# Performance work log

Measured on AMD Instinct MI355X. Metric: run time of the kernel, lower is better.

Reference implementation:

```python
import jax, jax.numpy as jnp
import numpy as np

CH, XH, YH, RADIUS = 2, 2, 2, 1  # channel_heads, x_heads, y_heads, neighborhood radius


def neighborhood_mask(n_sub_x, n_sub_y, radius):
    # clamped neighbor offsets reduce to |di|<=r and |dj|<=r within the grid
    iy = jnp.arange(n_sub_y)
    ix = jnp.arange(n_sub_x)
    my = jnp.abs(iy[:, None] - iy[None, :]) <= radius  # [ny, ny]
    mx = jnp.abs(ix[:, None] - ix[None, :]) <= radius  # [nx, nx]
    m = my[:, None, :, None] & mx[None, :, None, :]    # [ny, nx, ny, nx]
    s = n_sub_x * n_sub_y
    return m.reshape(s, s)  # row-major (h1 w1)(h2 w2), matching einops


def setup_inputs() -> dict:
    key = jax.random.key(0)
    k1, k2, k3 = jax.random.split(key, 3)
    C = 128
    seq = jax.random.normal(k1, (2, 256, C, 16, 16), dtype=jnp.float32)
    w_qkv = jax.random.normal(k2, (3 * C, C), dtype=jnp.float32) / np.sqrt(C).astype(np.float32)
    w_out = jax.random.normal(k3, (C, C), dtype=jnp.float32) / np.sqrt(C).astype(np.float32)
    b_out = jnp.zeros((C,), dtype=jnp.float32)
    return {"seq": seq, "w_qkv": w_qkv, "w_out": w_out, "b_out": b_out,
            "n_sub_x": 16, "n_sub_y": 16}


def reference(seq, w_qkv, w_out, b_out, n_sub_x, n_sub_y):
    b, s, C, H, W = seq.shape
    h, w = H // YH, W // XH
    c = C // CH
    nH = YH * XH * CH  # total heads

    # pointwise qkv projection over channels: [b, s, 3C, H, W]
    qkv = jnp.einsum('bschw,dc->bsdhw', seq, w_qkv)

    # decompose2d: split spatial grid into y_heads x x_heads blocks -> spatial heads
    # [b, s, 3C, YH, h, XH, w] -> [b, s, YH*XH, 3C, h, w]
    qkv = qkv.reshape(b, s, 3 * C, YH, h, XH, w)
    qkv = qkv.transpose(0, 1, 3, 5, 2, 4, 6).reshape(b, s, YH * XH, 3 * C, h, w)

    # split into q,k,v and channel heads: 3C = 3 * CH * c
    qkv = qkv.reshape(b, s, YH * XH, 3, CH, c, h, w)
    # -> [3, b, (spatial_heads * channel_heads), s, c, h, w]
    qkv = qkv.transpose(3, 0, 2, 4, 1, 5, 6, 7).reshape(3, b, nH, s, c, h, w)
    q, k, v = qkv[0], qkv[1], qkv[2]

    # scaled dot-product attention over flattened function dim (c,h,w)
    scale = 1.0 / np.sqrt(c * h * w).astype(np.float32)
    scores = jnp.einsum('bnschw,bntchw->bnst', q, k) * scale  # [b, nH, s, s]
    mask = neighborhood_mask(n_sub_x, n_sub_y, RADIUS)  # [s, s]
    scores = jnp.where(mask[None, None, :, :], scores, jnp.finfo(scores.dtype).min)
    attn = jax.nn.softmax(scores, axis=-1)
    sa = jnp.einsum('bnst,bntchw->bnschw', attn, v)  # [b, nH, s, c, h, w]

    # merge channel heads back: [b, s, spatial_heads, C, h, w]
    sa = sa.reshape(b, YH * XH, CH, s, c, h, w)
    sa = sa.transpose(0, 3, 1, 2, 4, 5, 6).reshape(b, s, YH, XH, C, h, w)
    # recompose2d: [b, s, C, H, W]
    sa = sa.transpose(0, 1, 4, 2, 5, 3, 6).reshape(b, s, C, H, W)

    # output pointwise projection with bias
    out = jnp.einsum('bschw,dc->bsdhw', sa, w_out) + b_out[None, None, :, None, None]
    return out
```

## Files before the change

kernel.cpp:

```cpp
#include <hip/hip_runtime.h>

#define BATCH 2
#define SS    256
#define CC    128
#define HWN   256
#define FDIM  4096

typedef unsigned int uint;
typedef unsigned short ushort;
typedef short bf16x8 __attribute__((ext_vector_type(8)));
typedef ushort us4 __attribute__((ext_vector_type(4)));
typedef float f32x4 __attribute__((ext_vector_type(4)));

__device__ __forceinline__ ushort f2b(float f) {
  uint u = __float_as_uint(f);
  return (ushort)((u + 0x7fffu + ((u >> 16) & 1u)) >> 16);
}
__device__ __forceinline__ float b2f(ushort h) { return __uint_as_float((uint)h << 16); }

__global__ void k_convert(const float* __restrict__ wqkv, const float* __restrict__ wout,
                          ushort* __restrict__ wqkv_b, ushort* __restrict__ wout_b) {
  int i = blockIdx.x * 256 + threadIdx.x;
  if (i < 384 * 128) wqkv_b[i] = f2b(wqkv[i]);
  if (i < 128 * 128) {
    const int cc = i & 127;
    const int ks = cc >> 5, qq = (cc >> 3) & 3, j = cc & 7;
    const int creal = (ks >> 1) * 64 + ((((ks & 1) << 1) | (qq >> 1)) << 4)
                      + ((qq & 1) << 3) + j;
    wout_b[i] = f2b(wout[(i >> 7) * 128 + creal]);
  }
}

__global__ __launch_bounds__(256, 2) void k_qkv(const float* __restrict__ seq,
                                                const ushort* __restrict__ wqkv_b,
                                                ushort* __restrict__ qkvh) {
  __shared__ ushort wlds[128 * 128];
  const int bs = blockIdx.x;
  const int b = bs >> 8, s = bs & 255;
  const int t = threadIdx.x;
  const int hq = t >> 6, lane = t & 63;
  const int qq = lane >> 4, m = lane & 15;

  const float* sp = seq + (size_t)bs * (CC * HWN);

  bf16x8 bfrag[4][4];
  uint obase[4];
  #pragma unroll
  for (int set = 0; set < 4; ++set) {
    const int ntg = hq * 4 + set;
    const int hw = ntg * 16 + m;
    #pragma unroll
    for (int ks = 0; ks < 4; ++ks) {
      const int k0 = ks * 32 + qq * 8;
      float tmp[8];
      #pragma unroll
      for (int j = 0; j < 8; ++j) tmp[j] = sp[(k0 + j) * HWN + hw];
      bf16x8 fr;
      #pragma unroll
      for (int j = 0; j < 8; ++j) fr[j] = (short)f2b(tmp[j]);
      bfrag[set][ks] = fr;
    }
    const int n_qk = ((ntg >> 3) * 2 + (m >> 3)) * 2;
    const int hwl  = (ntg & 7) * 8 + (m & 7);
    obase[set] = (uint)(((b * 8 + n_qk) * SS + s) * FDIM + hwl * 16 + qq * 4);
  }

  for (int qkvi = 0; qkvi < 3; ++qkvi) {
    if (qkvi) __syncthreads();
    #pragma unroll
    for (int i = 0; i < 8; ++i) {
      const int row = i * 16 + (t >> 4), col16 = t & 15;
      bf16x8 w = *(const bf16x8*)(wqkv_b + (qkvi * 128 + row) * 128 + col16 * 8);
      *(bf16x8*)&wlds[row * 128 + ((col16 ^ (row & 15)) * 8)] = w;
    }
    __syncthreads();

    #pragma unroll
    for (int mt8 = 0; mt8 < 8; ++mt8) {
      bf16x8 afrag[4];
      #pragma unroll
      for (int ks = 0; ks < 4; ++ks)
        afrag[ks] = *(const bf16x8*)&wlds[(mt8 * 16 + m) * 128 + (((ks * 4 + qq) ^ m) * 8)];
      const int ch = mt8 >> 2, m4 = mt8 & 3;
      #pragma unroll
      for (int set = 0; set < 4; ++set) {
        f32x4 acc = {0.f, 0.f, 0.f, 0.f};
        #pragma unroll
        for (int ks = 0; ks < 4; ++ks)
          acc = __builtin_amdgcn_mfma_f32_16x16x32_bf16(afrag[ks], bfrag[set][ks], acc, 0, 0, 0);
        us4 pk;
        #pragma unroll
        for (int r = 0; r < 4; ++r) pk[r] = f2b(acc[r]);
        *(us4*)(qkvh + obase[set]
                + (uint)((qkvi * 16 + ch) * (SS * FDIM) + m4 * 1024)) = pk;
      }
    }
  }
}

__global__ __launch_bounds__(1024) void k_scores(const ushort* __restrict__ qkvh,
                                                 float* __restrict__ attn) {
  __shared__ float red[16][64][12];
  const int g = blockIdx.x;
  const int unit = (g & 7) * 32 + (g >> 3);
  const int b  = unit >> 7;
  const int n  = (unit >> 4) & 7;
  const int sy = unit & 15;
  const int t = threadIdx.x;
  const int wave = t >> 6, lane = t & 63;
  const int qq = lane >> 4, l15 = lane & 15;
  const size_t hs = (size_t)SS * FDIM;
  const ushort* qb = qkvh + (size_t)(b * 8 + n) * hs;
  const ushort* kb = qkvh + (size_t)(16 + b * 8 + n) * hs;

  const ushort* qp = qb + (size_t)(sy * 16 + l15) * FDIM + qq * 8;
  const ushort* kp[3];
  #pragma unroll
  for (int tl = 0; tl < 3; ++tl) {
    const int tyc = min(max(sy - 1 + tl, 0), 15);
    kp[tl] = kb + (size_t)(tyc * 16 + l15) * FDIM + qq * 8;
  }

  f32x4 acc[3] = {{0,0,0,0},{0,0,0,0},{0,0,0,0}};
  const int kbeg = wave * 256;
  #pragma unroll
  for (int it = 0; it < 4; ++it) {
    const int k0 = kbeg + it * 64;
    bf16x8 a0 = *(const bf16x8*)(qp + k0);
    bf16x8 a1 = *(const bf16x8*)(qp + k0 + 32);
    bf16x8 b0[3], b1[3];
    #pragma unroll
    for (int tl = 0; tl < 3; ++tl) {
      b0[tl] = *(const bf16x8*)(kp[tl] + k0);
      b1[tl] = *(const bf16x8*)(kp[tl] + k0 + 32);
    }
    #pragma unroll
    for (int tl = 0; tl < 3; ++tl)
      acc[tl] = __builtin_amdgcn_mfma_f32_16x16x32_bf16(a0, b0[tl], acc[tl], 0, 0, 0);
    #pragma unroll
    for (int tl = 0; tl < 3; ++tl)
      acc[tl] = __builtin_amdgcn_mfma_f32_16x16x32_bf16(a1, b1[tl], acc[tl], 0, 0, 0);
  }

  #pragma unroll
  for (int tl = 0; tl < 3; ++tl)
    #pragma unroll
    for (int r = 0; r < 4; ++r) red[wave][lane][tl * 4 + r] = acc[tl][r];
  __syncthreads();
  if (t < 768) {
    const int lane2 = t / 12, idx = t - lane2 * 12;
    float ssum = red[0][lane2][idx];
    #pragma unroll
    for (int w = 1; w < 16; ++w) ssum += red[w][lane2][idx];
    red[0][lane2][idx] = ssum;
  }
  __syncthreads();
  if (wave != 0) return;
  #pragma unroll
  for (int tl = 0; tl < 3; ++tl)
    #pragma unroll
    for (int r = 0; r < 4; ++r) acc[tl][r] = red[0][lane][tl * 4 + r];

  const int tx = l15;
  float sc[3][4];
  #pragma unroll
  for (int tl = 0; tl < 3; ++tl) {
    const int ty = sy - 1 + tl;
    const bool tyv = (ty >= 0 && ty < 16);
    #pragma unroll
    for (int r = 0; r < 4; ++r) {
      const int sx = qq * 4 + r;
      const bool v = tyv && (tx - sx <= 1) && (sx - tx <= 1);
      sc[tl][r] = v ? acc[tl][r] * (1.f / 64.f) : -1e30f;
    }
  }
  #pragma unroll
  for (int r = 0; r < 4; ++r) {
    float mx = fmaxf(fmaxf(sc[0][r], sc[1][r]), sc[2][r]);
    #pragma unroll
    for (int off = 1; off < 16; off <<= 1) mx = fmaxf(mx, __shfl_xor(mx, off));
    float p[3], sum = 0.f;
    #pragma unroll
    for (int tl = 0; tl < 3; ++tl) { p[tl] = __expf(sc[tl][r] - mx); sum += p[tl]; }
    #pragma unroll
    for (int off = 1; off < 16; off <<= 1) sum += __shfl_xor(sum, off);
    const float inv = 1.f / sum;
    const int sx = qq * 4 + r;
    const int s = sy * 16 + sx;
    #pragma unroll
    for (int tl = 0; tl < 3; ++tl) {
      const int ty = sy - 1 + tl;
      const int dxp = tx - sx + 1;
      if (ty >= 0 && ty < 16 && dxp >= 0 && dxp <= 2)
        attn[((size_t)(b * 8 + n) * SS + s) * 9 + tl * 3 + dxp] = p[tl] * inv;
    }
  }
}

__global__ __launch_bounds__(256, 2) void k_out(const ushort* __restrict__ qkvh,
                                                const float* __restrict__ attn,
                                                const ushort* __restrict__ wout_b,
                                                const float* __restrict__ bout,
                                                float* __restrict__ out) {
  __shared__ ushort wlds[128 * 128];
  const int g = blockIdx.x;
  const int bs = (g & 7) * 64 + (g >> 3);
  const int b = bs >> 8, s = bs & 255;
  const int sy = s >> 4, sx = s & 15;
  const int t = threadIdx.x;
  const int sub = t >> 6, lane = t & 63;
  const int qq = lane >> 4, m = lane & 15;
  const size_t hs = (size_t)SS * FDIM;

  #pragma unroll
  for (int i = 0; i < 8; ++i) {
    const int row = i * 16 + (t >> 4), col16 = t & 15;
    bf16x8 w = *(const bf16x8*)(wout_b + row * 128 + col16 * 8);
    *(bf16x8*)&wlds[row * 128 + ((col16 ^ (row & 15)) * 8)] = w;
  }

  int sjc[9];
  bool vld[9];
  #pragma unroll
  for (int j = 0; j < 9; ++j) {
    const int ny = sy + j / 3 - 1, nx = sx + j % 3 - 1;
    vld[j] = (ny >= 0 && ny < 16 && nx >= 0 && nx < 16);
    sjc[j] = min(max(ny, 0), 15) * 16 + min(max(nx, 0), 15);
  }

  bf16x8 bfrag[4][4];
  #pragma unroll
  for (int set = 0; set < 4; ++set) {
    const int ntg = sub * 4 + set;
    const int nbase = ((ntg >> 3) * 2 + (m >> 3)) * 2;
    const int hwl = (ntg & 7) * 8 + (m & 7);

    float pch[2][9];
    #pragma unroll
    for (int ch = 0; ch < 2; ++ch) {
      #pragma unroll
      for (int j = 0; j < 9; ++j) {
        const float w = attn[((size_t)(b * 8 + nbase + ch) * SS + s) * 9 + j];
        pch[ch][j] = vld[j] ? w : 0.f;
      }
    }

    #pragma unroll
    for (int ks = 0; ks < 4; ++ks) {
      const int ch = ks >> 1;
      const int c64hi = ((ks & 1) << 1) | (qq >> 1);
      const int half = qq & 1;
      const ushort* vb = qkvh + (size_t)(32 + b * 8 + nbase + ch) * hs;
      const int off = c64hi * 1024 + hwl * 16 + half * 8;
      float facc[8] = {0.f, 0.f, 0.f, 0.f, 0.f, 0.f, 0.f, 0.f};
      #pragma unroll
      for (int j = 0; j < 9; ++j) {
        bf16x8 vv = *(const bf16x8*)(vb + (size_t)sjc[j] * FDIM + off);
        const float pj = pch[ch][j];
        #pragma unroll
        for (int e = 0; e < 8; ++e) facc[e] += pj * b2f((ushort)vv[e]);
      }
      bf16x8 fr;
      #pragma unroll
      for (int e = 0; e < 8; ++e) fr[e] = (short)f2b(facc[e]);
      bfrag[set][ks] = fr;
    }
  }

  __syncthreads();

  #pragma unroll
  for (int mt = 0; mt < 8; ++mt) {
    bf16x8 afrag[4];
    #pragma unroll
    for (int ks = 0; ks < 4; ++ks)
      afrag[ks] = *(const bf16x8*)&wlds[(mt * 16 + m) * 128 + (((ks * 4 + qq) ^ m) * 8)];
    #pragma unroll
    for (int set = 0; set < 4; ++set) {
      f32x4 acc = {0.f, 0.f, 0.f, 0.f};
      #pragma unroll
      for (int ks = 0; ks < 4; ++ks)
        acc = __builtin_amdgcn_mfma_f32_16x16x32_bf16(afrag[ks], bfrag[set][ks], acc, 0, 0, 0);
      const int hw = (sub * 4 + set) * 16 + m;
      #pragma unroll
      for (int r = 0; r < 4; ++r) {
        const int d = mt * 16 + qq * 4 + r;
        out[((size_t)bs * CC + d) * HWN + hw] = acc[r] + bout[d];
      }
    }
  }
}

extern "C" void kernel_launch(void* const* d_in, const int* in_sizes, int n_in,
                              void* d_out, int out_size, void* d_ws, size_t ws_size,
                              hipStream_t stream) {
  const float* seq  = (const float*)d_in[0];
  const float* wqkv = (const float*)d_in[1];
  const float* wout = (const float*)d_in[2];
  const float* bout = (const float*)d_in[3];
  char* ws = (char*)d_ws;
  ushort* wqkv_b = (ushort*)(ws);
  ushort* wout_b = (ushort*)(ws + 98304);
  ushort* qkvh   = (ushort*)(ws + 131072);
  float*  attn   = (float*)(ws + 131072 + 100663296ull);
  float*  outp   = (float*)d_out;

  hipLaunchKernelGGL(k_convert, dim3(192), dim3(256), 0, stream, wqkv, wout, wqkv_b, wout_b);
  hipLaunchKernelGGL(k_qkv,     dim3(512), dim3(256), 0, stream, seq, wqkv_b, qkvh);
  hipLaunchKernelGGL(k_scores,  dim3(256), dim3(1024), 0, stream, qkvh, attn);
  hipLaunchKernelGGL(k_out,     dim3(512), dim3(256), 0, stream, qkvh, attn, wout_b, bout, outp);
}
```

Before: 192.3 us.

## Split fused PV+projection kernel into separate PV and projection kernels

```diff
diff --git a/kernel.cpp b/kernel.cpp
--- a/kernel.cpp
+++ b/kernel.cpp
@@ -197,18 +197,69 @@
   }
 }
 
-__global__ __launch_bounds__(256, 2) void k_out(const ushort* __restrict__ qkvh,
-                                                const float* __restrict__ attn,
-                                                const ushort* __restrict__ wout_b,
-                                                const float* __restrict__ bout,
-                                                float* __restrict__ out) {
+__global__ __launch_bounds__(256) void k_pv(const ushort* __restrict__ qkvh,
+                                            const float* __restrict__ attn,
+                                            ushort* __restrict__ sa) {
+  const int g = blockIdx.x;
+  const int unit = (g & 7) * 512 + (g >> 3);
+  const int eta = unit >> 8, s = unit & 255;
+  const int sy = s >> 4, sx = s & 15;
+  const int t = threadIdx.x;
+  const size_t hs = (size_t)SS * FDIM;
+
+  float p[9];
+  int sjc[9];
+  bool vld[9];
+  #pragma unroll
+  for (int j = 0; j < 9; ++j) {
+    const int ny = sy + j / 3 - 1, nx = sx + j % 3 - 1;
+    vld[j] = (ny >= 0 && ny < 16 && nx >= 0 && nx < 16);
+    sjc[j] = min(max(ny, 0), 15) * 16 + min(max(nx, 0), 15);
+    p[j] = vld[j] ? attn[((size_t)eta * SS + s) * 9 + j] : 0.f;
+  }
+
+  const ushort* vb = qkvh + (size_t)(32 + eta) * hs;
+  const int f0 = t * 16;
+  float acc[16];
+  #pragma unroll
+  for (int e = 0; e < 16; ++e) acc[e] = 0.f;
+  #pragma unroll
+  for (int j = 0; j < 9; ++j) {
+    if (vld[j]) {
+      const ushort* vp = vb + (size_t)sjc[j] * FDIM + f0;
+      bf16x8 v0 = *(const bf16x8*)(vp);
+      bf16x8 v1 = *(const bf16x8*)(vp + 8);
+      const float pj = p[j];
+      #pragma unroll
+      for (int e = 0; e < 8; ++e) acc[e]     += pj * b2f((ushort)v0[e]);
+      #pragma unroll
+      for (int e = 0; e < 8; ++e) acc[8 + e] += pj * b2f((ushort)v1[e]);
+    }
+  }
+  bf16x8 r0, r1;
+  #pragma unroll
+  for (int e = 0; e < 8; ++e) { r0[e] = (short)f2b(acc[e]); r1[e] = (short)f2b(acc[8 + e]); }
+  ushort* op = sa + ((size_t)eta * SS + s) * FDIM + f0;
+  *(bf16x8*)op = r0;
+  *(bf16x8*)(op + 8) = r1;
+}
+
+__global__ __launch_bounds__(256) void k_proj(const ushort* __restrict__ qkvh,
+                                              const ushort* __restrict__ wout_b,
+                                              const float* __restrict__ bout,
+                                              float* __restrict__ out) {
   __shared__ ushort wlds[128 * 128];
   const int g = blockIdx.x;
-  const int bs = (g & 7) * 64 + (g >> 3);
-  const int b = bs >> 8, s = bs & 255;
-  const int sy = s >> 4, sx = s & 15;
+  const int r9 = g >> 3;
+  const int G = (g & 7) * 4 + (r9 >> 6);
+  const int idx = r9 & 63;
+  const int b = G >> 4, sy = G & 15;
+  const int sx = idx >> 2, sub = idx & 3;
+  const int s = sy * 16 + sx;
+  const int bs = b * 256 + s;
   const int t = threadIdx.x;
-  const int sub = t >> 6, lane = t & 63;
+  const int wave = t >> 6, lane = t & 63;
+  const int ntg = sub * 4 + wave;
   const int qq = lane >> 4, m = lane & 15;
   const size_t hs = (size_t)SS * FDIM;
 
@@ -219,52 +270,17 @@
     *(bf16x8*)&wlds[row * 128 + ((col16 ^ (row & 15)) * 8)] = w;
   }
 
-  int sjc[9];
-  bool vld[9];
-  #pragma unroll
-  for (int j = 0; j < 9; ++j) {
-    const int ny = sy + j / 3 - 1, nx = sx + j % 3 - 1;
-    vld[j] = (ny >= 0 && ny < 16 && nx >= 0 && nx < 16);
-    sjc[j] = min(max(ny, 0), 15) * 16 + min(max(nx, 0), 15);
-  }
-
-  bf16x8 bfrag[4][4];
-  #pragma unroll
-  for (int set = 0; set < 4; ++set) {
-    const int ntg = sub * 4 + set;
-    const int nbase = ((ntg >> 3) * 2 + (m >> 3)) * 2;
-    const int hwl = (ntg & 7) * 8 + (m & 7);
-
-    float pch[2][9];
-    #pragma unroll
-    for (int ch = 0; ch < 2; ++ch) {
-      #pragma unroll
-      for (int j = 0; j < 9; ++j) {
-        const float w = attn[((size_t)(b * 8 + nbase + ch) * SS + s) * 9 + j];
-        pch[ch][j] = vld[j] ? w : 0.f;
-      }
-    }
-
-    #pragma unroll
-    for (int ks = 0; ks < 4; ++ks) {
-      const int ch = ks >> 1;
-      const int c64hi = ((ks & 1) << 1) | (qq >> 1);
-      const int half = qq & 1;
-      const ushort* vb = qkvh + (size_t)(32 + b * 8 + nbase + ch) * hs;
-      const int off = c64hi * 1024 + hwl * 16 + half * 8;
-      float facc[8] = {0.f, 0.f, 0.f, 0.f, 0.f, 0.f, 0.f, 0.f};
-      #pragma unroll
-      for (int j = 0; j < 9; ++j) {
-        bf16x8 vv = *(const bf16x8*)(vb + (size_t)sjc[j] * FDIM + off);
-        const float pj = pch[ch][j];
-        #pragma unroll
-        for (int e = 0; e < 8; ++e) facc[e] += pj * b2f((ushort)vv[e]);
-      }
-      bf16x8 fr;
-      #pragma unroll
-      for (int e = 0; e < 8; ++e) fr[e] = (short)f2b(facc[e]);
-      bfrag[set][ks] = fr;
-    }
+  const int nbase = ((ntg >> 3) * 2 + (m >> 3)) * 2;
+  const int hwl = (ntg & 7) * 8 + (m & 7);
+  bf16x8 bfrag[4];
+  #pragma unroll
+  for (int ks = 0; ks < 4; ++ks) {
+    const int ch = ks >> 1;
+    const int c64hi = ((ks & 1) << 1) | (qq >> 1);
+    const int half = qq & 1;
+    const ushort* sb = qkvh + (size_t)(b * 8 + nbase + ch) * hs;
+    const int off = c64hi * 1024 + hwl * 16 + half * 8;
+    bfrag[ks] = *(const bf16x8*)(sb + (size_t)s * FDIM + off);
   }
 
   __syncthreads();
@@ -275,18 +291,15 @@
     #pragma unroll
     for (int ks = 0; ks < 4; ++ks)
       afrag[ks] = *(const bf16x8*)&wlds[(mt * 16 + m) * 128 + (((ks * 4 + qq) ^ m) * 8)];
-    #pragma unroll
-    for (int set = 0; set < 4; ++set) {
-      f32x4 acc = {0.f, 0.f, 0.f, 0.f};
-      #pragma unroll
-      for (int ks = 0; ks < 4; ++ks)
-        acc = __builtin_amdgcn_mfma_f32_16x16x32_bf16(afrag[ks], bfrag[set][ks], acc, 0, 0, 0);
-      const int hw = (sub * 4 + set) * 16 + m;
-      #pragma unroll
-      for (int r = 0; r < 4; ++r) {
-        const int d = mt * 16 + qq * 4 + r;
-        out[((size_t)bs * CC + d) * HWN + hw] = acc[r] + bout[d];
-      }
+    f32x4 acc = {0.f, 0.f, 0.f, 0.f};
+    #pragma unroll
+    for (int ks = 0; ks < 4; ++ks)
+      acc = __builtin_amdgcn_mfma_f32_16x16x32_bf16(afrag[ks], bfrag[ks], acc, 0, 0, 0);
+    const int hw = ntg * 16 + m;
+    #pragma unroll
+    for (int r = 0; r < 4; ++r) {
+      const int d = mt * 16 + qq * 4 + r;
+      out[((size_t)bs * CC + d) * HWN + hw] = acc[r] + bout[d];
     }
   }
 }
@@ -305,8 +318,9 @@
   float*  attn   = (float*)(ws + 131072 + 100663296ull);
   float*  outp   = (float*)d_out;
 
-  hipLaunchKernelGGL(k_convert, dim3(192), dim3(256), 0, stream, wqkv, wout, wqkv_b, wout_b);
-  hipLaunchKernelGGL(k_qkv,     dim3(512), dim3(256), 0, stream, seq, wqkv_b, qkvh);
-  hipLaunchKernelGGL(k_scores,  dim3(256), dim3(1024), 0, stream, qkvh, attn);
-  hipLaunchKernelGGL(k_out,     dim3(512), dim3(256), 0, stream, qkvh, attn, wout_b, bout, outp);
-}
+  hipLaunchKernelGGL(k_convert, dim3(192),  dim3(256), 0, stream, wqkv, wout, wqkv_b, wout_b);
+  hipLaunchKernelGGL(k_qkv,     dim3(512),  dim3(256), 0, stream, seq, wqkv_b, qkvh);
+  hipLaunchKernelGGL(k_scores,  dim3(256),  dim3(1024), 0, stream, qkvh, attn);
+  hipLaunchKernelGGL(k_pv,      dim3(4096), dim3(256), 0, stream, qkvh, attn, qkvh );
+  hipLaunchKernelGGL(k_proj,    dim3(2048), dim3(256), 0, stream, qkvh, wout_b, bout, outp);
+}
```

Result: no change. 195.2 us (+1.5%).
